# Kernel tuning notes

Measured on AMD Instinct MI355X. Metric: run time of the kernel, lower is better.

The kernel has to match this reference:

```python
import jax, jax.numpy as jnp
import numpy as np

N = 8192   # nodes per modality
D = 128    # hidden_channels
H = 2      # transformer heads
R = 15     # relations in HeteroConv (use_speaker='no')
E = 16384  # edges per relation
L = 2      # num_layers
# relation src/dst node-type ids: 0=audio, 1=text, 2=visual (dict order: a/v/t past, a/v/t future, a/v/t self, then cross)
SRC = np.array([0, 2, 1, 0, 2, 1, 0, 2, 1, 0, 0, 2, 2, 1, 1])
DST = np.array([0, 2, 1, 0, 2, 1, 0, 2, 1, 2, 1, 0, 1, 0, 2])


def setup_inputs() -> dict:
    key = jax.random.key(0)
    ks = jax.random.split(key, 18)
    f = lambda k, sh: jax.random.normal(k, sh, dtype=jnp.float32) * 0.05
    return {
        "x_audio": jax.random.normal(ks[0], (N, D), jnp.float32),
        "x_text": jax.random.normal(ks[1], (N, D), jnp.float32),
        "x_visual": jax.random.normal(ks[2], (N, D), jnp.float32),
        "edge_index": jax.random.randint(ks[3], (R, 2, E), 0, N, jnp.int32),
        "Wrel": f(ks[4], (L, R, D, D)),
        "brel": f(ks[5], (L, R, D)),
        "Wroot": f(ks[6], (L, R, D, D)),
        "Wq": f(ks[7], (D, H * D)), "bq": f(ks[8], (H * D,)),
        "Wk": f(ks[9], (D, H * D)), "bk": f(ks[10], (H * D,)),
        "Wv": f(ks[11], (D, H * D)), "bv": f(ks[12], (H * D,)),
        "Wskip": f(ks[13], (D, D)), "bskip": f(ks[14], (D,)),
        "gamma": jnp.ones((D,), jnp.float32),
        "beta": jnp.zeros((D,), jnp.float32),
    }


def reference(x_audio, x_text, x_visual, edge_index, Wrel, brel, Wroot,
              Wq, bq, Wk, bk, Wv, bv, Wskip, bskip, gamma, beta):
    src_t = jnp.asarray(SRC)
    dst_t = jnp.asarray(DST)
    x = jnp.stack([x_audio, x_text, x_visual])           # [3, N, D]
    src_idx = edge_index[:, 0]                            # [R, E]
    dst_idx = edge_index[:, 1]                            # [R, E]
    rel = jnp.arange(R)

    # --- HeteroConv of 15 GraphConvs (aggr='add' inside, 'mean' over the 5 relations per dst type) ---
    seg = (rel[:, None] * N + dst_idx).reshape(-1)        # per-relation segment ids
    for l in range(L):
        feats = jnp.take_along_axis(x[src_t], src_idx[:, :, None], axis=1)     # [R, E, D]
        msg = jax.ops.segment_sum(feats.reshape(R * E, D), seg,
                                  num_segments=R * N).reshape(R, N, D)          # scatter-add per relation
        out = (jnp.einsum('rnd,rde->rne', msg, Wrel[l]) + brel[l][:, None, :]
               + jnp.einsum('rnd,rde->rne', x[dst_t], Wroot[l]))                # lin_rel(agg) + lin_root(x_dst)
        x = jax.nn.relu(jnp.zeros_like(x).at[dst_t].add(out) / 5.0)            # mean over 5 relations per dst

    # --- hetero_to_homo: concat audio, text, visual (offsets 0, N, 2N) ---
    hx = x.reshape(3 * N, D)
    src_h = (src_t[:, None] * N + src_idx).reshape(-1)    # [R*E]
    dst_h = (dst_t[:, None] * N + dst_idx).reshape(-1)

    # --- TransformerConv (concat=False -> head mean, root skip) ---
    q = (hx @ Wq + bq).reshape(3 * N, H, D)
    k = (hx @ Wk + bk).reshape(3 * N, H, D)
    v = (hx @ Wv + bv).reshape(3 * N, H, D)
    logits = jnp.einsum('ehd,ehd->eh', q[dst_h], k[src_h]) / jnp.sqrt(jnp.float32(D))
    m = jax.ops.segment_max(logits, dst_h, num_segments=3 * N)
    p = jnp.exp(logits - m[dst_h])
    denom = jax.ops.segment_sum(p, dst_h, num_segments=3 * N)
    alpha = p / denom[dst_h]                              # segment softmax over incoming edges
    agg = jax.ops.segment_sum(alpha[:, :, None] * v[src_h], dst_h, num_segments=3 * N)  # [3N, H, D]
    out = agg.mean(axis=1) + hx @ Wskip + bskip

    # --- BatchNorm1d (training-mode batch stats) + leaky_relu ---
    mu = out.mean(axis=0)
    var = ((out - mu) ** 2).mean(axis=0)
    y = (out - mu) / jnp.sqrt(var + 1e-5) * gamma + beta
    y = jax.nn.leaky_relu(y)                              # negative_slope=0.01 (torch default)
    return y.reshape(3, N, D)                             # [audio, text, visual]
```

## Files before the change

### kernel.cpp

```cpp
#include <hip/hip_runtime.h>
#include <hip/hip_bf16.h>

#define NN 8192
#define DD 128
#define HH 2
#define RR 15
#define EE 16384
#define NLAYER 2
#define NMOD 3
#define TN (NMOD*NN)
#define NE (RR*EE)

#define SRC_BITS 0x16818618u
#define DST_BITS 0x21198618u
__device__ __forceinline__ int srcOf(int r) { return (SRC_BITS >> (2 * r)) & 3; }
__device__ __forceinline__ int dstOf(int r) { return (DST_BITS >> (2 * r)) & 3; }

typedef __attribute__((ext_vector_type(8))) short bf16x8;
typedef __attribute__((ext_vector_type(4))) float f32x4;
typedef _Float16 h2 __attribute__((ext_vector_type(2)));

__device__ __forceinline__ unsigned short f2bf(float v) {
    union { float f; unsigned int u; } x; x.f = v;
    unsigned int r = (x.u + 0x7fffu + ((x.u >> 16) & 1u)) >> 16;
    return (unsigned short)r;
}
__device__ __forceinline__ float bf2f(unsigned int bits16) {
    return __uint_as_float(bits16 << 16);
}
__device__ __forceinline__ void bfu4(uint4 u, float* f) {
    f[0] = bf2f(u.x & 0xffffu); f[1] = bf2f(u.x >> 16);
    f[2] = bf2f(u.y & 0xffffu); f[3] = bf2f(u.y >> 16);
    f[4] = bf2f(u.z & 0xffffu); f[5] = bf2f(u.z >> 16);
    f[6] = bf2f(u.w & 0xffffu); f[7] = bf2f(u.w >> 16);
}

__device__ __forceinline__ float dot8_f16(uint4 a, uint4 b, float acc) {
#if __has_builtin(__builtin_amdgcn_fdot2)
    acc = __builtin_amdgcn_fdot2(__builtin_bit_cast(h2, a.x), __builtin_bit_cast(h2, b.x), acc, false);
    acc = __builtin_amdgcn_fdot2(__builtin_bit_cast(h2, a.y), __builtin_bit_cast(h2, b.y), acc, false);
    acc = __builtin_amdgcn_fdot2(__builtin_bit_cast(h2, a.z), __builtin_bit_cast(h2, b.z), acc, false);
    acc = __builtin_amdgcn_fdot2(__builtin_bit_cast(h2, a.w), __builtin_bit_cast(h2, b.w), acc, false);
#else
    h2 av, bv;
    av = __builtin_bit_cast(h2, a.x); bv = __builtin_bit_cast(h2, b.x);
    acc += (float)av.x * (float)bv.x + (float)av.y * (float)bv.y;
    av = __builtin_bit_cast(h2, a.y); bv = __builtin_bit_cast(h2, b.y);
    acc += (float)av.x * (float)bv.x + (float)av.y * (float)bv.y;
    av = __builtin_bit_cast(h2, a.z); bv = __builtin_bit_cast(h2, b.z);
    acc += (float)av.x * (float)bv.x + (float)av.y * (float)bv.y;
    av = __builtin_bit_cast(h2, a.w); bv = __builtin_bit_cast(h2, b.w);
    acc += (float)av.x * (float)bv.x + (float)av.y * (float)bv.y;
#endif
    return acc;
}

__global__ __launch_bounds__(256) void prep_all(
        const float* __restrict__ Wrel, const float* __restrict__ Wroot,
        const float* __restrict__ brel,
        const float* __restrict__ Wq, const float* __restrict__ Wk,
        const float* __restrict__ Wv, const float* __restrict__ Wskip,
        const float* __restrict__ xa, const float* __restrict__ xt,
        const float* __restrict__ xv,
        unsigned short* __restrict__ WrelT, unsigned short* __restrict__ WsumT,
        float* __restrict__ bsum,
        unsigned short* __restrict__ WqT, unsigned short* __restrict__ WkT,
        unsigned short* __restrict__ WvT, unsigned short* __restrict__ WskipT,
        unsigned short* __restrict__ xb, int* __restrict__ cnt) {
    int y = blockIdx.y;
    int t = blockIdx.x * 256 + threadIdx.x;
    if (y < 30) {
        int k = t >> 7, c = t & 127;
        WrelT[(size_t)y * 16384 + c * 128 + k] = f2bf(Wrel[(size_t)y * 16384 + t]);
    } else if (y < 36) {
        int mat = y - 30, l = mat / 3, m = mat % 3;
        int k = t >> 7, c = t & 127;
        float s = 0.f;
        #pragma unroll
        for (int r = 0; r < RR; r++)
            if (((DST_BITS >> (2 * r)) & 3) == (unsigned)m) s += Wroot[(size_t)(l * RR + r) * 16384 + t];
        WsumT[(size_t)mat * 16384 + c * 128 + k] = f2bf(s);
        if (blockIdx.x == 0 && threadIdx.x < 128) {
            float b = 0.f;
            #pragma unroll
            for (int r = 0; r < RR; r++)
                if (((DST_BITS >> (2 * r)) & 3) == (unsigned)m) b += brel[(l * RR + r) * 128 + threadIdx.x];
            bsum[mat * 128 + threadIdx.x] = b;
        }
    } else if (y < 39) {
        int which = y - 36;
        const float* s = which == 0 ? Wq : which == 1 ? Wk : Wv;
        unsigned short* d = which == 0 ? WqT : which == 1 ? WkT : WvT;
        #pragma unroll
        for (int it = 0; it < 2; it++) {
            int tt = t + it * 16384;
            int k = tt >> 8, c = tt & 255;
            d[c * 128 + k] = f2bf(s[tt]);
        }
    } else if (y == 39) {
        int k = t >> 7, c = t & 127;
        WskipT[c * 128 + k] = f2bf(Wskip[t]);
    } else if (y == 40) {
        for (int i = t; i < TN + 256; i += 16384) cnt[i] = 0;
    } else {
        int m = y - 41;
        const float* s = m == 0 ? xa : m == 1 ? xt : xv;
        unsigned short* d = xb + (size_t)m * NN * DD;
        for (int i = t * 4; i < NN * DD; i += 16384 * 4) {
            float4 v = *(const float4*)(s + i);
            uint2 o;
            o.x = (unsigned)f2bf(v.x) | ((unsigned)f2bf(v.y) << 16);
            o.y = (unsigned)f2bf(v.z) | ((unsigned)f2bf(v.w) << 16);
            *(uint2*)(d + i) = o;
        }
    }
}

__global__ void count_edges(const int* __restrict__ edge, int* __restrict__ cnt) {
    int t = blockIdx.x * 256 + threadIdx.x;
    if (t >= NE) return;
    int r = t >> 14, e = t & (EE - 1);
    int dst = edge[r * 2 * EE + EE + e];
    atomicAdd(&cnt[dstOf(r) * NN + dst], 1);
}

__global__ void scan_kernel(const int* __restrict__ cnt, int* __restrict__ startA,
                            int* __restrict__ cursor) {
    __shared__ int part[1024];
    int t = threadIdx.x;
    int base = t * (TN / 1024);
    int s = 0;
    for (int i = 0; i < TN / 1024; i++) s += cnt[base + i];
    part[t] = s;
    __syncthreads();
    for (int ofs = 1; ofs < 1024; ofs <<= 1) {
        int v = (t >= ofs) ? part[t - ofs] : 0;
        __syncthreads();
        part[t] += v;
        __syncthreads();
    }
    int run = (t == 0) ? 0 : part[t - 1];
    for (int i = 0; i < TN / 1024; i++) {
        startA[base + i] = run;
        cursor[base + i] = run;
        run += cnt[base + i];
    }
    if (t == 1023) startA[TN] = part[1023];
}

__global__ void place_edges(const int* __restrict__ edge, int* __restrict__ cursor,
                            unsigned int* __restrict__ sorted) {
    int t = blockIdx.x * 256 + threadIdx.x;
    if (t >= NE) return;
    int r = t >> 14, e = t & (EE - 1);
    int src = edge[r * 2 * EE + e];
    int dst = edge[r * 2 * EE + EE + e];
    int pos = atomicAdd(&cursor[dstOf(r) * NN + dst], 1);
    unsigned int zrow = ((unsigned int)r << 13) | (unsigned int)src;
    unsigned int srch = (unsigned int)(srcOf(r) * NN + src);
    sorted[pos] = (zrow << 15) | srch;
}

template<int MODE>
__device__ __forceinline__ void gemm_tile(const unsigned short* __restrict__ A,
                                          const unsigned short* __restrict__ BT,
                                          const float* __restrict__ bias,
                                          void* __restrict__ Cout,
                                          int ldc, int colofs, int row0,
                                          unsigned short* lds, float oscale = 1.f) {
    unsigned short* Alds = lds;
    unsigned short* Blds = lds + 16384;
    const int tid = threadIdx.x;
    const int lane = tid & 63;
    const int w = tid >> 6;
    #pragma unroll
    for (int i = 0; i < 8; i++) {
        int c = i * 256 + tid;
        int row = c >> 4;
        int k0 = (c & 15) << 3;
        uint4 va = *(const uint4*)(A + (size_t)(row0 + row) * 128 + k0);
        *(uint4*)((char*)Alds + (((row * 256 + k0 * 2)) ^ ((row & 7) << 4))) = va;
        uint4 vb = *(const uint4*)(BT + (size_t)row * 128 + k0);
        *(uint4*)((char*)Blds + (((row * 256 + k0 * 2)) ^ ((row & 7) << 4))) = vb;
    }
    __syncthreads();
    f32x4 acc[2][8];
    #pragma unroll
    for (int mi = 0; mi < 2; mi++)
        #pragma unroll
        for (int nj = 0; nj < 8; nj++) acc[mi][nj] = (f32x4){0.f, 0.f, 0.f, 0.f};
    const int lr = lane & 15, lk = lane >> 4;
    #pragma unroll
    for (int ks = 0; ks < 4; ks++) {
        bf16x8 a[2], b[8];
        #pragma unroll
        for (int mi = 0; mi < 2; mi++) {
            int row = w * 32 + mi * 16 + lr;
            a[mi] = *(const bf16x8*)((char*)Alds + ((row * 256 + (ks * 32 + lk * 8) * 2) ^ ((row & 7) << 4)));
        }
        #pragma unroll
        for (int nj = 0; nj < 8; nj++) {
            int row = nj * 16 + lr;
            b[nj] = *(const bf16x8*)((char*)Blds + ((row * 256 + (ks * 32 + lk * 8) * 2) ^ ((row & 7) << 4)));
        }
        #pragma unroll
        for (int mi = 0; mi < 2; mi++)
            #pragma unroll
            for (int nj = 0; nj < 8; nj++)
                acc[mi][nj] = __builtin_amdgcn_mfma_f32_16x16x32_bf16(a[mi], b[nj], acc[mi][nj], 0, 0, 0);
    }
    __syncthreads();
    float* Clds = (float*)lds;
    #pragma unroll
    for (int mi = 0; mi < 2; mi++) {
        #pragma unroll
        for (int nj = 0; nj < 8; nj++) {
            int ccl = nj * 16 + lr;
            float bb = bias ? bias[ccl] : 0.f;
            #pragma unroll
            for (int r = 0; r < 4; r++) {
                int row = w * 32 + mi * 16 + lk * 4 + r;
                Clds[row * 128 + ccl] = acc[mi][nj][r] + bb;
            }
        }
    }
    __syncthreads();
    #pragma unroll
    for (int p = 0; p < 8; p++) {
        int row = p * 16 + (tid >> 4);
        int c0 = (tid & 15) * 8;
        float4 fa = *(const float4*)(Clds + row * 128 + c0);
        float4 fb = *(const float4*)(Clds + row * 128 + c0 + 4);
        if (MODE == 2) {
            unsigned r0 = (unsigned)f2bf(fa.x) | ((unsigned)f2bf(fa.y) << 16);
            unsigned r1 = (unsigned)f2bf(fa.z) | ((unsigned)f2bf(fa.w) << 16);
            unsigned r2 = (unsigned)f2bf(fb.x) | ((unsigned)f2bf(fb.y) << 16);
            unsigned r3 = (unsigned)f2bf(fb.z) | ((unsigned)f2bf(fb.w) << 16);
            uint4 pk = {r0, r1, r2, r3};
            *(uint4*)((unsigned short*)Cout + (size_t)(row0 + row) * ldc + colofs + c0) = pk;
        } else if (MODE == 3) {
            unsigned r0 = __builtin_bit_cast(unsigned, __builtin_amdgcn_cvt_pkrtz(fa.x * oscale, fa.y * oscale));
            unsigned r1 = __builtin_bit_cast(unsigned, __builtin_amdgcn_cvt_pkrtz(fa.z * oscale, fa.w * oscale));
            unsigned r2 = __builtin_bit_cast(unsigned, __builtin_amdgcn_cvt_pkrtz(fb.x * oscale, fb.y * oscale));
            unsigned r3 = __builtin_bit_cast(unsigned, __builtin_amdgcn_cvt_pkrtz(fb.z * oscale, fb.w * oscale));
            uint4 pk = {r0, r1, r2, r3};
            *(uint4*)((unsigned short*)Cout + (size_t)(row0 + row) * ldc + colofs + c0) = pk;
        } else {
            float* Cf = (float*)Cout;
            *(float4*)(Cf + (size_t)(row0 + row) * ldc + colofs + c0) = fa;
            *(float4*)(Cf + (size_t)(row0 + row) * ldc + colofs + c0 + 4) = fb;
        }
    }
}

__global__ __launch_bounds__(256) void zroot_gemm(const unsigned short* __restrict__ xbf,
                                                  const unsigned short* __restrict__ WrelT_l,
                                                  const unsigned short* __restrict__ WrootSumT_l,
                                                  const float* __restrict__ brelSum_l,
                                                  unsigned short* __restrict__ z,
                                                  unsigned short* __restrict__ xroot) {
    __shared__ unsigned short lds[2 * 16384];
    int y = blockIdx.y;
    if (y < RR) {
        gemm_tile<2>(xbf + (size_t)srcOf(y) * NN * 128, WrelT_l + (size_t)y * 16384, nullptr,
                     z + (size_t)y * NN * 128, 128, 0, blockIdx.x * 128, lds);
    } else {
        int m = y - RR;
        gemm_tile<2>(xbf + (size_t)m * NN * 128, WrootSumT_l + (size_t)m * 16384, brelSum_l + m * 128,
                     xroot + (size_t)m * NN * 128, 128, 0, blockIdx.x * 128, lds);
    }
}

__global__ __launch_bounds__(256) void qkvskip_gemm(const unsigned short* __restrict__ xbf,
                                                    const unsigned short* __restrict__ WqT,
                                                    const unsigned short* __restrict__ WkT,
                                                    const unsigned short* __restrict__ WvT,
                                                    const unsigned short* __restrict__ WskipT,
                                                    const float* __restrict__ bq,
                                                    const float* __restrict__ bk,
                                                    const float* __restrict__ bv,
                                                    const float* __restrict__ bskip,
                                                    unsigned short* __restrict__ qb,
                                                    unsigned short* __restrict__ kb,
                                                    unsigned short* __restrict__ vb,
                                                    float* __restrict__ out) {
    __shared__ unsigned short lds[2 * 16384];
    int y = blockIdx.y;
    if (y < 4) {
        int which = y >> 1, half = y & 1;
        const unsigned short* BT = (which == 0 ? WqT : WkT) + half * 16384;
        const float* bias = (which == 0 ? bq : bk) + half * 128;
        unsigned short* C = (which == 0 ? qb : kb);
        float os = (which == 0) ? 0.08838834764831845f : 1.f;
        gemm_tile<3>(xbf, BT, bias, C, 256, half * 128, blockIdx.x * 128, lds, os);
    } else if (y < 6) {
        int half = y & 1;
        gemm_tile<2>(xbf, WvT + half * 16384, bv + half * 128, vb, 256, half * 128, blockIdx.x * 128, lds);
    } else {
        gemm_tile<0>(xbf, WskipT, bskip, out, 128, 0, blockIdx.x * 128, lds);
    }
}

__global__ __launch_bounds__(256) void gather_relu(const unsigned short* __restrict__ z,
                                                   const unsigned short* __restrict__ xroot,
                                                   const unsigned int* __restrict__ sorted,
                                                   const int* __restrict__ startA,
                                                   unsigned short* __restrict__ xout) {
    int node = blockIdx.x * 4 + (threadIdx.x >> 6);
    int lane = threadIdx.x & 63;
    int g = lane >> 4, p = lane & 15;
    int st = startA[node], en = startA[node + 1];
    float acc[8];
    #pragma unroll
    for (int j = 0; j < 8; j++) acc[j] = 0.f;
    int idx = st + g;
    unsigned int vcur = (idx < en) ? sorted[idx] : 0u;
    for (int base = st; base < en; base += 4) {
        unsigned int vnext = (idx + 4 < en) ? sorted[idx + 4] : 0u;
        uint4 u = *(const uint4*)(z + ((size_t)(vcur >> 15) << 7) + p * 8);
        if (idx < en) {
            float f[8]; bfu4(u, f);
            #pragma unroll
            for (int j = 0; j < 8; j++) acc[j] += f[j];
        }
        vcur = vnext;
        idx += 4;
    }
    #pragma unroll
    for (int j = 0; j < 8; j++) {
        acc[j] += __shfl_xor(acc[j], 32);
        acc[j] += __shfl_xor(acc[j], 16);
    }
    if (g == 0) {
        uint4 rt = *(const uint4*)(xroot + ((size_t)node << 7) + p * 8);
        float r[8]; bfu4(rt, r);
        unsigned short o[8];
        #pragma unroll
        for (int j = 0; j < 8; j++) {
            float v = (r[j] + acc[j]) * 0.2f;
            o[j] = f2bf(v > 0.f ? v : 0.f);
        }
        uint4 pk;
        pk.x = (unsigned)o[0] | ((unsigned)o[1] << 16);
        pk.y = (unsigned)o[2] | ((unsigned)o[3] << 16);
        pk.z = (unsigned)o[4] | ((unsigned)o[5] << 16);
        pk.w = (unsigned)o[6] | ((unsigned)o[7] << 16);
        *(uint4*)(xout + ((size_t)node << 7) + p * 8) = pk;
    }
}

__global__ __launch_bounds__(256) void attn_fused(const unsigned short* __restrict__ qb,
                                                  const unsigned short* __restrict__ kb,
                                                  const unsigned short* __restrict__ vb,
                                                  const unsigned int* __restrict__ sorted,
                                                  const int* __restrict__ startA,
                                                  float* __restrict__ out) {
    int node = blockIdx.x * 4 + (threadIdx.x >> 6);
    int lane = threadIdx.x & 63;
    int g = lane >> 4, p = lane & 15;
    uint4 q0 = *(const uint4*)(qb + (size_t)node * 256 + p * 8);
    uint4 q1 = *(const uint4*)(qb + (size_t)node * 256 + 128 + p * 8);
    float s0 = 0.f, s1 = 0.f;
    float a0[8], a1[8];
    #pragma unroll
    for (int j = 0; j < 8; j++) { a0[j] = 0.f; a1[j] = 0.f; }
    int st = startA[node], en = startA[node + 1];
    int idx = st + g;
    unsigned int vcur = (idx < en) ? sorted[idx] : 0u;
    for (int base = st; base < en; base += 4) {
        unsigned int vnext = (idx + 4 < en) ? sorted[idx + 4] : 0u;
        bool valid = idx < en;
        int srch = (int)(vcur & 32767u);
        const unsigned short* krow = kb + (size_t)srch * 256;
        const unsigned short* vrow = vb + (size_t)srch * 256;
        uint4 k0r = *(const uint4*)(krow + p * 8);
        uint4 k1r = *(const uint4*)(krow + 128 + p * 8);
        uint4 v0r = *(const uint4*)(vrow + p * 8);
        uint4 v1r = *(const uint4*)(vrow + 128 + p * 8);
        float d0 = dot8_f16(q0, k0r, 0.f);
        float d1 = dot8_f16(q1, k1r, 0.f);
        #pragma unroll
        for (int off = 8; off >= 1; off >>= 1) {
            d0 += __shfl_xor(d0, off);
            d1 += __shfl_xor(d1, off);
        }
        float p0 = valid ? __expf(d0) : 0.f;
        float p1 = valid ? __expf(d1) : 0.f;
        s0 += p0; s1 += p1;
        float v0[8], v1[8];
        bfu4(v0r, v0); bfu4(v1r, v1);
        #pragma unroll
        for (int j = 0; j < 8; j++) {
            a0[j] += p0 * v0[j];
            a1[j] += p1 * v1[j];
        }
        vcur = vnext;
        idx += 4;
    }
    #pragma unroll
    for (int off = 32; off >= 16; off >>= 1) {
        s0 += __shfl_xor(s0, off);
        s1 += __shfl_xor(s1, off);
        #pragma unroll
        for (int j = 0; j < 8; j++) {
            a0[j] += __shfl_xor(a0[j], off);
            a1[j] += __shfl_xor(a1[j], off);
        }
    }
    if (g == 0) {
        float inv0 = (s0 > 0.f) ? 0.5f / s0 : 0.f;
        float inv1 = (s1 > 0.f) ? 0.5f / s1 : 0.f;
        float* op = out + (size_t)node * 128 + p * 8;
        float4 ska = *(const float4*)op;
        float4 skb = *(const float4*)(op + 4);
        float4 ra, rb;
        ra.x = a0[0] * inv0 + a1[0] * inv1 + ska.x;
        ra.y = a0[1] * inv0 + a1[1] * inv1 + ska.y;
        ra.z = a0[2] * inv0 + a1[2] * inv1 + ska.z;
        ra.w = a0[3] * inv0 + a1[3] * inv1 + ska.w;
        rb.x = a0[4] * inv0 + a1[4] * inv1 + skb.x;
        rb.y = a0[5] * inv0 + a1[5] * inv1 + skb.y;
        rb.z = a0[6] * inv0 + a1[6] * inv1 + skb.z;
        rb.w = a0[7] * inv0 + a1[7] * inv1 + skb.w;
        *(float4*)op = ra;
        *(float4*)(op + 4) = rb;
    }
}

__global__ void colstats(const float* __restrict__ outb, float* __restrict__ stats) {
    int col = threadIdx.x & 127;
    int sub = threadIdx.x >> 7;
    float s = 0.f, ss = 0.f;
    for (int row = blockIdx.x * 2 + sub; row < TN; row += gridDim.x * 2) {
        float vv = outb[(size_t)row * DD + col];
        s += vv;
        ss += vv * vv;
    }
    __shared__ float red[2][256];
    red[0][threadIdx.x] = s;
    red[1][threadIdx.x] = ss;
    __syncthreads();
    if (sub == 0) {
        s  += red[0][threadIdx.x + 128];
        ss += red[1][threadIdx.x + 128];
        atomicAdd(&stats[col], s);
        atomicAdd(&stats[DD + col], ss);
    }
}

__global__ void ln_act(float* __restrict__ outb, const float* __restrict__ stats,
                       const float* __restrict__ gamma, const float* __restrict__ beta) {
    int i = (blockIdx.x * 256 + threadIdx.x) * 4;
    if (i >= TN * DD) return;
    int col = i & 127;
    float4 v = *(const float4*)(outb + i);
    float o[4] = {v.x, v.y, v.z, v.w};
    #pragma unroll
    for (int j = 0; j < 4; j++) {
        int c = col + j;
        float mu = stats[c] * (1.f / TN);
        float var = stats[DD + c] * (1.f / TN) - mu * mu;
        float inv = rsqrtf(var + 1e-5f);
        float vv = (o[j] - mu) * inv * gamma[c] + beta[c];
        o[j] = vv > 0.f ? vv : 0.01f * vv;
    }
    float4 res = {o[0], o[1], o[2], o[3]};
    *(float4*)(outb + i) = res;
}

extern "C" void kernel_launch(void* const* d_in, const int* in_sizes, int n_in,
                              void* d_out, int out_size, void* d_ws, size_t ws_size,
                              hipStream_t stream) {
    const float* x_audio = (const float*)d_in[0];
    const float* x_text  = (const float*)d_in[1];
    const float* x_vis   = (const float*)d_in[2];
    const int*   edge    = (const int*)d_in[3];
    const float* Wrel    = (const float*)d_in[4];
    const float* brel    = (const float*)d_in[5];
    const float* Wroot   = (const float*)d_in[6];
    const float* Wq      = (const float*)d_in[7];
    const float* bq      = (const float*)d_in[8];
    const float* Wk      = (const float*)d_in[9];
    const float* bk      = (const float*)d_in[10];
    const float* Wv      = (const float*)d_in[11];
    const float* bv      = (const float*)d_in[12];
    const float* Wskip   = (const float*)d_in[13];
    const float* bskip   = (const float*)d_in[14];
    const float* gamma   = (const float*)d_in[15];
    const float* beta    = (const float*)d_in[16];
    float* out = (float*)d_out;

    char* p = (char*)d_ws;
    unsigned short* xbfA = (unsigned short*)p; p += (size_t)TN * 128 * 2;
    unsigned short* xbfB = (unsigned short*)p; p += (size_t)TN * 128 * 2;
    unsigned short* zqkv = (unsigned short*)p; p += (size_t)3 * TN * 256 * 2;
    unsigned short* z  = zqkv;
    unsigned short* qb = zqkv;
    unsigned short* kb = zqkv + (size_t)TN * 256;
    unsigned short* vb = zqkv + (size_t)2 * TN * 256;
    unsigned short* xroot = (unsigned short*)p; p += (size_t)TN * 128 * 2;
    unsigned short* WrelT = (unsigned short*)p; p += (size_t)2 * RR * 16384 * 2;
    unsigned short* WrootSumT = (unsigned short*)p; p += (size_t)6 * 16384 * 2;
    float* brelSum = (float*)p; p += 6 * 128 * 4;
    unsigned short* WqT = (unsigned short*)p; p += 256 * 128 * 2;
    unsigned short* WkT = (unsigned short*)p; p += 256 * 128 * 2;
    unsigned short* WvT = (unsigned short*)p; p += 256 * 128 * 2;
    unsigned short* WskipT = (unsigned short*)p; p += 128 * 128 * 2;
    unsigned int* sorted = (unsigned int*)p; p += (size_t)NE * 4;
    int* startA = (int*)p; p += (TN + 1) * 4;
    int* cursor = (int*)p; p += (TN + 1) * 4;
    int* cnt = (int*)p; p += TN * 4;
    float* stats = (float*)p; p += 256 * 4;
    size_t needed = (size_t)(p - (char*)d_ws);
    if (ws_size < needed) return;

    prep_all<<<dim3(64, 44), 256, 0, stream>>>(Wrel, Wroot, brel, Wq, Wk, Wv, Wskip,
                                               x_audio, x_text, x_vis,
                                               WrelT, WrootSumT, brelSum,
                                               WqT, WkT, WvT, WskipT, xbfA, cnt);

    count_edges<<<NE / 256, 256, 0, stream>>>(edge, cnt);
    scan_kernel<<<1, 1024, 0, stream>>>(cnt, startA, cursor);
    place_edges<<<NE / 256, 256, 0, stream>>>(edge, cursor, sorted);

    unsigned short* xcur = xbfA;
    unsigned short* xnxt = xbfB;
    for (int l = 0; l < NLAYER; ++l) {
        zroot_gemm<<<dim3(NN / 128, RR + NMOD), 256, 0, stream>>>(
            xcur, WrelT + (size_t)l * RR * 16384, WrootSumT + (size_t)l * NMOD * 16384,
            brelSum + l * NMOD * 128, z, xroot);
        gather_relu<<<TN / 4, 256, 0, stream>>>(z, xroot, sorted, startA, xnxt);
        unsigned short* t = xcur; xcur = xnxt; xnxt = t;
    }

    qkvskip_gemm<<<dim3(TN / 128, 7), 256, 0, stream>>>(xcur, WqT, WkT, WvT, WskipT,
                                                        bq, bk, bv, bskip, qb, kb, vb, out);
    attn_fused<<<TN / 4, 256, 0, stream>>>(qb, kb, vb, sorted, startA, out);

    colstats<<<384, 256, 0, stream>>>(out, stats);
    ln_act<<<(TN * DD) / 1024, 256, 0, stream>>>(out, stats, gamma, beta);
}
```

Before: 207.2 us.

## Aggregate-then-transform GraphConv via per-relation buckets and concatenated-K GEMM

Reorders each GraphConv layer so that raw bf16 source features are first summed per (destination node, relation slot) into a 768-wide message row, and then multiplied once by a concatenated [5 relation weights | summed root weight] matrix. This replaces the old approach of transforming all 15 relations' source features before gathering. The edge sort now buckets by destination and relation slot, and the scan is vectorized. It removes the 15 per-relation GEMMs and the large z buffer, in exchange for a wider-K GEMM and a gather that runs one 64-lane row per bucket serially. The attention value accumulation also moves to packed fp16 arithmetic, and V is now stored as fp16 to match, which risks precision loss in the accumulation.

```diff
diff --git a/kernel.cpp b/kernel.cpp
--- a/kernel.cpp
+++ b/kernel.cpp
@@ -10,6 +10,7 @@
 #define NMOD 3
 #define TN (NMOD*NN)
 #define NE (RR*EE)
+#define NB (TN*5)
 
 #define SRC_BITS 0x16818618u
 #define DST_BITS 0x21198618u
@@ -27,12 +28,6 @@
 }
 __device__ __forceinline__ float bf2f(unsigned int bits16) {
     return __uint_as_float(bits16 << 16);
-}
-__device__ __forceinline__ void bfu4(uint4 u, float* f) {
-    f[0] = bf2f(u.x & 0xffffu); f[1] = bf2f(u.x >> 16);
-    f[2] = bf2f(u.y & 0xffffu); f[3] = bf2f(u.y >> 16);
-    f[4] = bf2f(u.z & 0xffffu); f[5] = bf2f(u.z >> 16);
-    f[6] = bf2f(u.w & 0xffffu); f[7] = bf2f(u.w >> 16);
 }
 
 __device__ __forceinline__ float dot8_f16(uint4 a, uint4 b, float acc) {
@@ -55,6 +50,10 @@
     return acc;
 }
 
+__device__ __forceinline__ h2 h2shfl_xor(h2 a, int off) {
+    return __builtin_bit_cast(h2, __shfl_xor(__builtin_bit_cast(int, a), off));
+}
+
 __global__ __launch_bounds__(256) void prep_all(
         const float* __restrict__ Wrel, const float* __restrict__ Wroot,
         const float* __restrict__ brel,
@@ -62,30 +61,34 @@
         const float* __restrict__ Wv, const float* __restrict__ Wskip,
         const float* __restrict__ xa, const float* __restrict__ xt,
         const float* __restrict__ xv,
-        unsigned short* __restrict__ WrelT, unsigned short* __restrict__ WsumT,
-        float* __restrict__ bsum,
+        unsigned short* __restrict__ WcatT, float* __restrict__ bsum,
         unsigned short* __restrict__ WqT, unsigned short* __restrict__ WkT,
         unsigned short* __restrict__ WvT, unsigned short* __restrict__ WskipT,
         unsigned short* __restrict__ xb, int* __restrict__ cnt) {
     int y = blockIdx.y;
     int t = blockIdx.x * 256 + threadIdx.x;
-    if (y < 30) {
-        int k = t >> 7, c = t & 127;
-        WrelT[(size_t)y * 16384 + c * 128 + k] = f2bf(Wrel[(size_t)y * 16384 + t]);
-    } else if (y < 36) {
-        int mat = y - 30, l = mat / 3, m = mat % 3;
-        int k = t >> 7, c = t & 127;
-        float s = 0.f;
-        #pragma unroll
-        for (int r = 0; r < RR; r++)
-            if (((DST_BITS >> (2 * r)) & 3) == (unsigned)m) s += Wroot[(size_t)(l * RR + r) * 16384 + t];
-        WsumT[(size_t)mat * 16384 + c * 128 + k] = f2bf(s);
-        if (blockIdx.x == 0 && threadIdx.x < 128) {
-            float b = 0.f;
+    if (y < 36) {
+        int mat = y / 6, j = y - mat * 6;
+        int l = mat / 3, m = mat - l * 3;
+        int k = t >> 7, oc = t & 127;
+        unsigned short* W = WcatT + (size_t)mat * 128 * 768;
+        if (j < 5) {
+            int r = 3 * j;
+            while (((DST_BITS >> (2 * r)) & 3) != (unsigned)m) r++;
+            W[(size_t)oc * 768 + j * 128 + k] = f2bf(Wrel[(size_t)(l * RR + r) * 16384 + t]);
+        } else {
+            float s = 0.f;
             #pragma unroll
             for (int r = 0; r < RR; r++)
-                if (((DST_BITS >> (2 * r)) & 3) == (unsigned)m) b += brel[(l * RR + r) * 128 + threadIdx.x];
-            bsum[mat * 128 + threadIdx.x] = b;
+                if (((DST_BITS >> (2 * r)) & 3) == (unsigned)m) s += Wroot[(size_t)(l * RR + r) * 16384 + t];
+            W[(size_t)oc * 768 + 640 + k] = f2bf(s);
+            if (blockIdx.x == 0 && threadIdx.x < 128) {
+                float b = 0.f;
+                #pragma unroll
+                for (int r = 0; r < RR; r++)
+                    if (((DST_BITS >> (2 * r)) & 3) == (unsigned)m) b += brel[(l * RR + r) * 128 + threadIdx.x];
+                bsum[mat * 128 + threadIdx.x] = b;
+            }
         }
     } else if (y < 39) {
         int which = y - 36;
@@ -101,7 +104,7 @@
         int k = t >> 7, c = t & 127;
         WskipT[c * 128 + k] = f2bf(Wskip[t]);
     } else if (y == 40) {
-        for (int i = t; i < TN + 256; i += 16384) cnt[i] = 0;
+        for (int i = t; i < NB + 256; i += 16384) cnt[i] = 0;
     } else {
         int m = y - 41;
         const float* s = m == 0 ? xa : m == 1 ? xt : xv;
@@ -121,16 +124,19 @@
     if (t >= NE) return;
     int r = t >> 14, e = t & (EE - 1);
     int dst = edge[r * 2 * EE + EE + e];
-    atomicAdd(&cnt[dstOf(r) * NN + dst], 1);
-}
-
-__global__ void scan_kernel(const int* __restrict__ cnt, int* __restrict__ startA,
+    atomicAdd(&cnt[(dstOf(r) * NN + dst) * 5 + r / 3], 1);
+}
+
+__global__ void scan_kernel(const int* __restrict__ cnt, int* __restrict__ bs,
                             int* __restrict__ cursor) {
     __shared__ int part[1024];
     int t = threadIdx.x;
-    int base = t * (TN / 1024);
+    int base = t * (NB / 1024);
     int s = 0;
-    for (int i = 0; i < TN / 1024; i++) s += cnt[base + i];
+    for (int i = 0; i < NB / 1024; i += 4) {
+        int4 c = *(const int4*)(cnt + base + i);
+        s += c.x + c.y + c.z + c.w;
+    }
     part[t] = s;
     __syncthreads();
     for (int ofs = 1; ofs < 1024; ofs <<= 1) {
@@ -140,12 +146,17 @@
         __syncthreads();
     }
     int run = (t == 0) ? 0 : part[t - 1];
-    for (int i = 0; i < TN / 1024; i++) {
-        startA[base + i] = run;
-        cursor[base + i] = run;
-        run += cnt[base + i];
-    }
-    if (t == 1023) startA[TN] = part[1023];
+    for (int i = 0; i < NB / 1024; i += 4) {
+        int4 c = *(const int4*)(cnt + base + i);
+        int4 o;
+        o.x = run; run += c.x;
+        o.y = run; run += c.y;
+        o.z = run; run += c.z;
+        o.w = run; run += c.w;
+        *(int4*)(bs + base + i) = o;
+        *(int4*)(cursor + base + i) = o;
+    }
+    if (t == 1023) bs[NB] = part[1023];
 }
 
 __global__ void place_edges(const int* __restrict__ edge, int* __restrict__ cursor,
@@ -155,10 +166,112 @@
     int r = t >> 14, e = t & (EE - 1);
     int src = edge[r * 2 * EE + e];
     int dst = edge[r * 2 * EE + EE + e];
-    int pos = atomicAdd(&cursor[dstOf(r) * NN + dst], 1);
-    unsigned int zrow = ((unsigned int)r << 13) | (unsigned int)src;
-    unsigned int srch = (unsigned int)(srcOf(r) * NN + src);
-    sorted[pos] = (zrow << 15) | srch;
+    int pos = atomicAdd(&cursor[(dstOf(r) * NN + dst) * 5 + r / 3], 1);
+    sorted[pos] = (unsigned int)(srcOf(r) * NN + src);
+}
+
+__global__ __launch_bounds__(256) void gather_msg(const unsigned short* __restrict__ x,
+                                                  const unsigned int* __restrict__ sorted,
+                                                  const int* __restrict__ bs,
+                                                  unsigned short* __restrict__ msg) {
+    int h = blockIdx.x * 4 + (threadIdx.x >> 6);
+    int lane = threadIdx.x & 63;
+    const unsigned int* x32 = (const unsigned int*)x;
+    unsigned int* mrow = (unsigned int*)(msg + (size_t)h * 768);
+    int base = h * 5;
+    int st = bs[base];
+    #pragma unroll
+    for (int j = 0; j < 5; j++) {
+        int nx = bs[base + j + 1];
+        float a0 = 0.f, a1 = 0.f;
+        for (int e = st; e < nx; e++) {
+            unsigned int u = x32[(size_t)sorted[e] * 64 + lane];
+            a0 += bf2f(u & 0xffffu);
+            a1 += bf2f(u >> 16);
+        }
+        mrow[j * 64 + lane] = (unsigned)f2bf(a0) | ((unsigned)f2bf(a1) << 16);
+        st = nx;
+    }
+    mrow[320 + lane] = x32[(size_t)h * 64 + lane];
+}
+
+__global__ __launch_bounds__(256) void layer_gemm(const unsigned short* __restrict__ msg,
+                                                  const unsigned short* __restrict__ WcatT_l,
+                                                  const float* __restrict__ bsum_l,
+                                                  unsigned short* __restrict__ xnxt) {
+    __shared__ unsigned short lds[24576];
+    unsigned short* Alds = lds;
+    unsigned short* Blds = lds + 8192;
+    const int m = blockIdx.y;
+    const int row0 = blockIdx.x * 64;
+    const unsigned short* A = msg + ((size_t)m * NN + row0) * 768;
+    const unsigned short* BT = WcatT_l + (size_t)m * 128 * 768;
+    const int tid = threadIdx.x, lane = tid & 63, w = tid >> 6;
+    const int lr = lane & 15, lk = lane >> 4;
+    f32x4 acc[8];
+    #pragma unroll
+    for (int nj = 0; nj < 8; nj++) acc[nj] = (f32x4){0.f, 0.f, 0.f, 0.f};
+    #pragma unroll 1
+    for (int kc = 0; kc < 6; kc++) {
+        __syncthreads();
+        #pragma unroll
+        for (int i = 0; i < 4; i++) {
+            int c = i * 256 + tid;
+            int row = c >> 4, k0 = (c & 15) << 3;
+            uint4 va = *(const uint4*)(A + (size_t)row * 768 + kc * 128 + k0);
+            *(uint4*)((char*)Alds + ((row * 256 + k0 * 2) ^ ((row & 7) << 4))) = va;
+        }
+        #pragma unroll
+        for (int i = 0; i < 8; i++) {
+            int c = i * 256 + tid;
+            int row = c >> 4, k0 = (c & 15) << 3;
+            uint4 vb = *(const uint4*)(BT + (size_t)row * 768 + kc * 128 + k0);
+            *(uint4*)((char*)Blds + ((row * 256 + k0 * 2) ^ ((row & 7) << 4))) = vb;
+        }
+        __syncthreads();
+        #pragma unroll
+        for (int ks = 0; ks < 4; ks++) {
+            int arow = w * 16 + lr;
+            bf16x8 a = *(const bf16x8*)((char*)Alds + ((arow * 256 + (ks * 32 + lk * 8) * 2) ^ ((arow & 7) << 4)));
+            bf16x8 b[8];
+            #pragma unroll
+            for (int nj = 0; nj < 8; nj++) {
+                int brow = nj * 16 + lr;
+                b[nj] = *(const bf16x8*)((char*)Blds + ((brow * 256 + (ks * 32 + lk * 8) * 2) ^ ((brow & 7) << 4)));
+            }
+            #pragma unroll
+            for (int nj = 0; nj < 8; nj++)
+                acc[nj] = __builtin_amdgcn_mfma_f32_16x16x32_bf16(a, b[nj], acc[nj], 0, 0, 0);
+        }
+    }
+    __syncthreads();
+    float* Clds = (float*)lds;
+    #pragma unroll
+    for (int nj = 0; nj < 8; nj++) {
+        int col = nj * 16 + lr;
+        float bb = bsum_l[m * 128 + col];
+        #pragma unroll
+        for (int r = 0; r < 4; r++) {
+            int row = w * 16 + lk * 4 + r;
+            float v = (acc[nj][r] + bb) * 0.2f;
+            Clds[row * 128 + col] = v > 0.f ? v : 0.f;
+        }
+    }
+    __syncthreads();
+    unsigned short* X = xnxt + ((size_t)m * NN + row0) * 128;
+    #pragma unroll
+    for (int i = 0; i < 4; i++) {
+        int c = i * 256 + tid;
+        int row = c >> 4, c0 = (c & 15) * 8;
+        float4 fa = *(const float4*)(Clds + row * 128 + c0);
+        float4 fb = *(const float4*)(Clds + row * 128 + c0 + 4);
+        uint4 pk;
+        pk.x = (unsigned)f2bf(fa.x) | ((unsigned)f2bf(fa.y) << 16);
+        pk.y = (unsigned)f2bf(fa.z) | ((unsigned)f2bf(fa.w) << 16);
+        pk.z = (unsigned)f2bf(fb.x) | ((unsigned)f2bf(fb.y) << 16);
+        pk.w = (unsigned)f2bf(fb.z) | ((unsigned)f2bf(fb.w) << 16);
+        *(uint4*)(X + (size_t)row * 128 + c0) = pk;
+    }
 }
 
 template<int MODE>
@@ -231,14 +344,7 @@
         int c0 = (tid & 15) * 8;
         float4 fa = *(const float4*)(Clds + row * 128 + c0);
         float4 fb = *(const float4*)(Clds + row * 128 + c0 + 4);
-        if (MODE == 2) {
-            unsigned r0 = (unsigned)f2bf(fa.x) | ((unsigned)f2bf(fa.y) << 16);
-            unsigned r1 = (unsigned)f2bf(fa.z) | ((unsigned)f2bf(fa.w) << 16);
-            unsigned r2 = (unsigned)f2bf(fb.x) | ((unsigned)f2bf(fb.y) << 16);
-            unsigned r3 = (unsigned)f2bf(fb.z) | ((unsigned)f2bf(fb.w) << 16);
-            uint4 pk = {r0, r1, r2, r3};
-            *(uint4*)((unsigned short*)Cout + (size_t)(row0 + row) * ldc + colofs + c0) = pk;
-        } else if (MODE == 3) {
+        if (MODE == 3) {
             unsigned r0 = __builtin_bit_cast(unsigned, __builtin_amdgcn_cvt_pkrtz(fa.x * oscale, fa.y * oscale));
             unsigned r1 = __builtin_bit_cast(unsigned, __builtin_amdgcn_cvt_pkrtz(fa.z * oscale, fa.w * oscale));
             unsigned r2 = __builtin_bit_cast(unsigned, __builtin_amdgcn_cvt_pkrtz(fb.x * oscale, fb.y * oscale));
@@ -250,24 +356,6 @@
             *(float4*)(Cf + (size_t)(row0 + row) * ldc + colofs + c0) = fa;
             *(float4*)(Cf + (size_t)(row0 + row) * ldc + colofs + c0 + 4) = fb;
         }
-    }
-}
-
-__global__ __launch_bounds__(256) void zroot_gemm(const unsigned short* __restrict__ xbf,
-                                                  const unsigned short* __restrict__ WrelT_l,
-                                                  const unsigned short* __restrict__ WrootSumT_l,
-                                                  const float* __restrict__ brelSum_l,
-                                                  unsigned short* __restrict__ z,
-                                                  unsigned short* __restrict__ xroot) {
-    __shared__ unsigned short lds[2 * 16384];
-    int y = blockIdx.y;
-    if (y < RR) {
-        gemm_tile<2>(xbf + (size_t)srcOf(y) * NN * 128, WrelT_l + (size_t)y * 16384, nullptr,
-                     z + (size_t)y * NN * 128, 128, 0, blockIdx.x * 128, lds);
-    } else {
-        int m = y - RR;
-        gemm_tile<2>(xbf + (size_t)m * NN * 128, WrootSumT_l + (size_t)m * 16384, brelSum_l + m * 128,
-                     xroot + (size_t)m * NN * 128, 128, 0, blockIdx.x * 128, lds);
     }
 }
 
@@ -286,66 +374,15 @@
                                                     float* __restrict__ out) {
     __shared__ unsigned short lds[2 * 16384];
     int y = blockIdx.y;
-    if (y < 4) {
+    if (y < 6) {
         int which = y >> 1, half = y & 1;
-        const unsigned short* BT = (which == 0 ? WqT : WkT) + half * 16384;
-        const float* bias = (which == 0 ? bq : bk) + half * 128;
-        unsigned short* C = (which == 0 ? qb : kb);
+        const unsigned short* BT = (which == 0 ? WqT : which == 1 ? WkT : WvT) + half * 16384;
+        const float* bias = (which == 0 ? bq : which == 1 ? bk : bv) + half * 128;
+        unsigned short* C = (which == 0 ? qb : which == 1 ? kb : vb);
         float os = (which == 0) ? 0.08838834764831845f : 1.f;
         gemm_tile<3>(xbf, BT, bias, C, 256, half * 128, blockIdx.x * 128, lds, os);
-    } else if (y < 6) {
-        int half = y & 1;
-        gemm_tile<2>(xbf, WvT + half * 16384, bv + half * 128, vb, 256, half * 128, blockIdx.x * 128, lds);
     } else {
         gemm_tile<0>(xbf, WskipT, bskip, out, 128, 0, blockIdx.x * 128, lds);
-    }
-}
-
-__global__ __launch_bounds__(256) void gather_relu(const unsigned short* __restrict__ z,
-                                                   const unsigned short* __restrict__ xroot,
-                                                   const unsigned int* __restrict__ sorted,
-                                                   const int* __restrict__ startA,
-                                                   unsigned short* __restrict__ xout) {
-    int node = blockIdx.x * 4 + (threadIdx.x >> 6);
-    int lane = threadIdx.x & 63;
-    int g = lane >> 4, p = lane & 15;
-    int st = startA[node], en = startA[node + 1];
-    float acc[8];
-    #pragma unroll
-    for (int j = 0; j < 8; j++) acc[j] = 0.f;
-    int idx = st + g;
-    unsigned int vcur = (idx < en) ? sorted[idx] : 0u;
-    for (int base = st; base < en; base += 4) {
-        unsigned int vnext = (idx + 4 < en) ? sorted[idx + 4] : 0u;
-        uint4 u = *(const uint4*)(z + ((size_t)(vcur >> 15) << 7) + p * 8);
-        if (idx < en) {
-            float f[8]; bfu4(u, f);
-            #pragma unroll
-            for (int j = 0; j < 8; j++) acc[j] += f[j];
-        }
-        vcur = vnext;
-        idx += 4;
-    }
-    #pragma unroll
-    for (int j = 0; j < 8; j++) {
-        acc[j] += __shfl_xor(acc[j], 32);
-        acc[j] += __shfl_xor(acc[j], 16);
-    }
-    if (g == 0) {
-        uint4 rt = *(const uint4*)(xroot + ((size_t)node << 7) + p * 8);
-        float r[8]; bfu4(rt, r);
-        unsigned short o[8];
-        #pragma unroll
-        for (int j = 0; j < 8; j++) {
-            float v = (r[j] + acc[j]) * 0.2f;
-            o[j] = f2bf(v > 0.f ? v : 0.f);
-        }
-        uint4 pk;
-        pk.x = (unsigned)o[0] | ((unsigned)o[1] << 16);
-        pk.y = (unsigned)o[2] | ((unsigned)o[3] << 16);
-        pk.z = (unsigned)o[4] | ((unsigned)o[5] << 16);
-        pk.w = (unsigned)o[6] | ((unsigned)o[7] << 16);
-        *(uint4*)(xout + ((size_t)node << 7) + p * 8) = pk;
     }
 }
 
@@ -353,7 +390,7 @@
                                                   const unsigned short* __restrict__ kb,
                                                   const unsigned short* __restrict__ vb,
                                                   const unsigned int* __restrict__ sorted,
-                                                  const int* __restrict__ startA,
+                                                  const int* __restrict__ bs,
                                                   float* __restrict__ out) {
     int node = blockIdx.x * 4 + (threadIdx.x >> 6);
     int lane = threadIdx.x & 63;
@@ -361,18 +398,17 @@
     uint4 q0 = *(const uint4*)(qb + (size_t)node * 256 + p * 8);
     uint4 q1 = *(const uint4*)(qb + (size_t)node * 256 + 128 + p * 8);
     float s0 = 0.f, s1 = 0.f;
-    float a0[8], a1[8];
-    #pragma unroll
-    for (int j = 0; j < 8; j++) { a0[j] = 0.f; a1[j] = 0.f; }
-    int st = startA[node], en = startA[node + 1];
+    h2 a0h[4], a1h[4];
+    #pragma unroll
+    for (int jj = 0; jj < 4; jj++) { a0h[jj] = (h2){0, 0}; a1h[jj] = (h2){0, 0}; }
+    int st = bs[node * 5], en = bs[node * 5 + 5];
     int idx = st + g;
     unsigned int vcur = (idx < en) ? sorted[idx] : 0u;
     for (int base = st; base < en; base += 4) {
         unsigned int vnext = (idx + 4 < en) ? sorted[idx + 4] : 0u;
         bool valid = idx < en;
-        int srch = (int)(vcur & 32767u);
-        const unsigned short* krow = kb + (size_t)srch * 256;
-        const unsigned short* vrow = vb + (size_t)srch * 256;
+        const unsigned short* krow = kb + (size_t)vcur * 256;
+        const unsigned short* vrow = vb + (size_t)vcur * 256;
         uint4 k0r = *(const uint4*)(krow + p * 8);
         uint4 k1r = *(const uint4*)(krow + 128 + p * 8);
         uint4 v0r = *(const uint4*)(vrow + p * 8);
@@ -387,13 +423,16 @@
         float p0 = valid ? __expf(d0) : 0.f;
         float p1 = valid ? __expf(d1) : 0.f;
         s0 += p0; s1 += p1;
-        float v0[8], v1[8];
-        bfu4(v0r, v0); bfu4(v1r, v1);
-        #pragma unroll
-        for (int j = 0; j < 8; j++) {
-            a0[j] += p0 * v0[j];
-            a1[j] += p1 * v1[j];
-        }
+        h2 ph0 = (h2){(_Float16)p0, (_Float16)p0};
+        h2 ph1 = (h2){(_Float16)p1, (_Float16)p1};
+        a0h[0] += ph0 * __builtin_bit_cast(h2, v0r.x);
+        a0h[1] += ph0 * __builtin_bit_cast(h2, v0r.y);
+        a0h[2] += ph0 * __builtin_bit_cast(h2, v0r.z);
+        a0h[3] += ph0 * __builtin_bit_cast(h2, v0r.w);
+        a1h[0] += ph1 * __builtin_bit_cast(h2, v1r.x);
+        a1h[1] += ph1 * __builtin_bit_cast(h2, v1r.y);
+        a1h[2] += ph1 * __builtin_bit_cast(h2, v1r.z);
+        a1h[3] += ph1 * __builtin_bit_cast(h2, v1r.w);
         vcur = vnext;
         idx += 4;
     }
@@ -402,14 +441,20 @@
         s0 += __shfl_xor(s0, off);
         s1 += __shfl_xor(s1, off);
         #pragma unroll
-        for (int j = 0; j < 8; j++) {
-            a0[j] += __shfl_xor(a0[j], off);
-            a1[j] += __shfl_xor(a1[j], off);
+        for (int jj = 0; jj < 4; jj++) {
+            a0h[jj] += h2shfl_xor(a0h[jj], off);
+            a1h[jj] += h2shfl_xor(a1h[jj], off);
         }
     }
     if (g == 0) {
         float inv0 = (s0 > 0.f) ? 0.5f / s0 : 0.f;
         float inv1 = (s1 > 0.f) ? 0.5f / s1 : 0.f;
+        float a0[8], a1[8];
+        #pragma unroll
+        for (int jj = 0; jj < 4; jj++) {
+            a0[2 * jj] = (float)a0h[jj].x; a0[2 * jj + 1] = (float)a0h[jj].y;
+            a1[2 * jj] = (float)a1h[jj].x; a1[2 * jj + 1] = (float)a1h[jj].y;
+        }
         float* op = out + (size_t)node * 128 + p * 8;
         float4 ska = *(const float4*)op;
         float4 skb = *(const float4*)(op + 4);
@@ -493,49 +538,45 @@
     char* p = (char*)d_ws;
     unsigned short* xbfA = (unsigned short*)p; p += (size_t)TN * 128 * 2;
     unsigned short* xbfB = (unsigned short*)p; p += (size_t)TN * 128 * 2;
-    unsigned short* zqkv = (unsigned short*)p; p += (size_t)3 * TN * 256 * 2;
-    unsigned short* z  = zqkv;
-    unsigned short* qb = zqkv;
-    unsigned short* kb = zqkv + (size_t)TN * 256;
-    unsigned short* vb = zqkv + (size_t)2 * TN * 256;
-    unsigned short* xroot = (unsigned short*)p; p += (size_t)TN * 128 * 2;
-    unsigned short* WrelT = (unsigned short*)p; p += (size_t)2 * RR * 16384 * 2;
-    unsigned short* WrootSumT = (unsigned short*)p; p += (size_t)6 * 16384 * 2;
+    unsigned short* msg = (unsigned short*)p; p += (size_t)TN * 768 * 2;
+    unsigned short* qb = msg;
+    unsigned short* kb = msg + (size_t)TN * 256;
+    unsigned short* vb = msg + (size_t)2 * TN * 256;
+    unsigned short* WcatT = (unsigned short*)p; p += (size_t)6 * 128 * 768 * 2;
     float* brelSum = (float*)p; p += 6 * 128 * 4;
     unsigned short* WqT = (unsigned short*)p; p += 256 * 128 * 2;
     unsigned short* WkT = (unsigned short*)p; p += 256 * 128 * 2;
     unsigned short* WvT = (unsigned short*)p; p += 256 * 128 * 2;
     unsigned short* WskipT = (unsigned short*)p; p += 128 * 128 * 2;
     unsigned int* sorted = (unsigned int*)p; p += (size_t)NE * 4;
-    int* startA = (int*)p; p += (TN + 1) * 4;
-    int* cursor = (int*)p; p += (TN + 1) * 4;
-    int* cnt = (int*)p; p += TN * 4;
+    int* bs = (int*)p; p += (size_t)(NB + 4) * 4;
+    int* cursor = (int*)p; p += (size_t)NB * 4;
+    int* cnt = (int*)p; p += (size_t)NB * 4;
     float* stats = (float*)p; p += 256 * 4;
     size_t needed = (size_t)(p - (char*)d_ws);
     if (ws_size < needed) return;
 
     prep_all<<<dim3(64, 44), 256, 0, stream>>>(Wrel, Wroot, brel, Wq, Wk, Wv, Wskip,
                                                x_audio, x_text, x_vis,
-                                               WrelT, WrootSumT, brelSum,
+                                               WcatT, brelSum,
                                                WqT, WkT, WvT, WskipT, xbfA, cnt);
 
     count_edges<<<NE / 256, 256, 0, stream>>>(edge, cnt);
-    scan_kernel<<<1, 1024, 0, stream>>>(cnt, startA, cursor);
+    scan_kernel<<<1, 1024, 0, stream>>>(cnt, bs, cursor);
     place_edges<<<NE / 256, 256, 0, stream>>>(edge, cursor, sorted);
 
     unsigned short* xcur = xbfA;
     unsigned short* xnxt = xbfB;
     for (int l = 0; l < NLAYER; ++l) {
-        zroot_gemm<<<dim3(NN / 128, RR + NMOD), 256, 0, stream>>>(
-            xcur, WrelT + (size_t)l * RR * 16384, WrootSumT + (size_t)l * NMOD * 16384,
-            brelSum + l * NMOD * 128, z, xroot);
-        gather_relu<<<TN / 4, 256, 0, stream>>>(z, xroot, sorted, startA, xnxt);
+        gather_msg<<<TN / 4, 256, 0, stream>>>(xcur, sorted, bs, msg);
+        layer_gemm<<<dim3(NN / 64, NMOD), 256, 0, stream>>>(
+            msg, WcatT + (size_t)l * NMOD * 128 * 768, brelSum + l * NMOD * 128, xnxt);
         unsigned short* t = xcur; xcur = xnxt; xnxt = t;
     }
 
     qkvskip_gemm<<<dim3(TN / 128, 7), 256, 0, stream>>>(xcur, WqT, WkT, WvT, WskipT,
                                                         bq, bk, bv, bskip, qb, kb, vb, out);
-    attn_fused<<<TN / 4, 256, 0, stream>>>(qb, kb, vb, sorted, startA, out);
+    attn_fused<<<TN / 4, 256, 0, stream>>>(qb, kb, vb, sorted, bs, out);
 
     colstats<<<384, 256, 0, stream>>>(out, stats);
     ln_act<<<(TN * DD) / 1024, 256, 0, stream>>>(out, stats, gamma, beta);
```

Measured after the change: 283.4 us. 1.37x slower.
